# Kernel optimization log

Measured on AMD Instinct MI355X. Metric: run time of the kernel, lower is better.

The kernel has to match this reference:

```python
import jax, jax.numpy as jnp
import numpy as np

IMAGE_SIZE = 800.0          # torchvision default min_size
SCORE_THRESH = 0.25         # box_score_thresh from __init__
NMS_THRESH = 0.5            # box_nms_thresh from __init__
MAX_DET = 100               # torchvision detections_per_img default
BBOX_XFORM_CLIP = float(np.log(1000.0 / 16.0))  # torchvision BoxCoder clamp


def setup_inputs() -> dict:
    key = jax.random.key(0)
    k = jax.random.split(key, 5)
    B, N, D, C = 16, 4000, 1024, 2
    feats = jax.random.normal(k[0], (B, N, D), dtype=jnp.float32)
    # valid proposal boxes (x1,y1,x2,y2) inside the image
    cxcy = jax.random.uniform(k[1], (B, N, 2), minval=64.0, maxval=IMAGE_SIZE - 64.0)
    wh = jax.random.uniform(k[2], (B, N, 2), minval=16.0, maxval=128.0)
    proposals = jnp.concatenate([cxcy - wh * 0.5, cxcy + wh * 0.5], axis=-1)
    W_cls = jax.random.normal(k[3], (C, D), dtype=jnp.float32) * 0.02
    b_cls = jnp.zeros((C,), jnp.float32)
    W_box = jax.random.normal(k[4], (C * 4, D), dtype=jnp.float32) * 0.01
    b_box = jnp.zeros((C * 4,), jnp.float32)
    return dict(feats=feats, proposals=proposals, W_cls=W_cls, b_cls=b_cls,
                W_box=W_box, b_box=b_box)


def _decode_boxes(deltas, proposals):
    # torchvision BoxCoder with weights (10, 10, 5, 5)
    wx, wy, ww, wh = 10.0, 10.0, 5.0, 5.0
    widths = proposals[..., 2] - proposals[..., 0]
    heights = proposals[..., 3] - proposals[..., 1]
    ctr_x = proposals[..., 0] + 0.5 * widths
    ctr_y = proposals[..., 1] + 0.5 * heights
    dx = deltas[..., 0] / wx
    dy = deltas[..., 1] / wy
    dw = jnp.minimum(deltas[..., 2] / ww, BBOX_XFORM_CLIP)
    dh = jnp.minimum(deltas[..., 3] / wh, BBOX_XFORM_CLIP)
    pcx = dx * widths + ctr_x
    pcy = dy * heights + ctr_y
    pw = jnp.exp(dw) * widths
    ph = jnp.exp(dh) * heights
    boxes = jnp.stack([pcx - 0.5 * pw, pcy - 0.5 * ph,
                       pcx + 0.5 * pw, pcy + 0.5 * ph], axis=-1)
    return jnp.clip(boxes, 0.0, IMAGE_SIZE)


def _nms_keep(boxes, scores):
    # greedy NMS for one image; boxes [N,4], scores [N] (already thresholded)
    areas = jnp.maximum(boxes[:, 2] - boxes[:, 0], 0.0) * \
            jnp.maximum(boxes[:, 3] - boxes[:, 1], 0.0)

    def body(carry, _):
        s, keep = carry
        i = jnp.argmax(s)
        valid = s[i] > 0.0
        bi = boxes[i]
        ix1 = jnp.maximum(bi[0], boxes[:, 0])
        iy1 = jnp.maximum(bi[1], boxes[:, 1])
        ix2 = jnp.minimum(bi[2], boxes[:, 2])
        iy2 = jnp.minimum(bi[3], boxes[:, 3])
        inter = jnp.maximum(ix2 - ix1, 0.0) * jnp.maximum(iy2 - iy1, 0.0)
        iou = inter / (areas[i] + areas - inter + 1e-9)
        s = jnp.where(iou > NMS_THRESH, 0.0, s).at[i].set(0.0)
        keep = keep.at[i].set(valid)
        return (s, keep), None

    init = (scores, jnp.zeros(scores.shape, dtype=bool))
    (_, keep), _ = jax.lax.scan(body, init, None, length=MAX_DET)
    return keep


def reference(feats, proposals, W_cls, b_cls, W_box, b_box):
    logits = jnp.einsum('bnd,cd->bnc', feats, W_cls) + b_cls       # [B,N,2]
    deltas = jnp.einsum('bnd,ed->bne', feats, W_box) + b_box       # [B,N,8]
    probs = jax.nn.softmax(logits, axis=-1)
    scores = probs[..., 1]                                          # foreground class
    fg_deltas = deltas[..., 4:8]                                    # class-1 deltas
    boxes = _decode_boxes(fg_deltas, proposals)                     # [B,N,4]
    scores = jnp.where(scores > SCORE_THRESH, scores, 0.0)
    keep = jax.vmap(_nms_keep)(boxes, scores)                       # [B,N] bool
    final_scores = scores * keep.astype(scores.dtype)
    return jnp.concatenate([boxes, final_scores[..., None]], axis=-1)  # [B,N,5]
```

## Files before the change

kernel.cpp:

```cpp
#include <hip/hip_runtime.h>
#include <math.h>

#define IMG 800.0f
#define SCORE_TH 0.25f
#define NMS_TH 0.5f
#define MAXDET 100
#define BBOX_CLIP 4.135166556742356f

constexpr int kB = 16;
constexpr int kN = 4000;
constexpr int kD = 1024;

__global__ __launch_bounds__(256, 2) void head_kernel(
    const float* __restrict__ feats, const float* __restrict__ proposals,
    const float* __restrict__ Wc, const float* __restrict__ bc,
    const float* __restrict__ Wb, const float* __restrict__ bb,
    float* __restrict__ out, float* __restrict__ ws_scores,
    float* __restrict__ ws_boxes) {
  const int lane = threadIdx.x & 63;
  const int waveId = (blockIdx.x * blockDim.x + threadIdx.x) >> 6;
  const int nWaves = (gridDim.x * blockDim.x) >> 6;

  const float4* Wc4 = (const float4*)Wc;
  const float4* Wb4 = (const float4*)Wb;
  float4 w0[4], w1[4], w4[4], w5[4], w6[4], w7[4];
#pragma unroll
  for (int ch = 0; ch < 4; ++ch) {
    int idx = ch * 64 + lane;
    w0[ch] = Wc4[0 * 256 + idx];
    w1[ch] = Wc4[1 * 256 + idx];
    w4[ch] = Wb4[4 * 256 + idx];
    w5[ch] = Wb4[5 * 256 + idx];
    w6[ch] = Wb4[6 * 256 + idx];
    w7[ch] = Wb4[7 * 256 + idx];
  }
  const float bc0 = bc[0], bc1 = bc[1];
  const float bb4 = bb[4], bb5 = bb[5], bb6 = bb[6], bb7 = bb[7];

  const int R = kB * kN;
  for (int row = waveId; row < R; row += nWaves) {
    const float4* F = (const float4*)(feats + (size_t)row * kD);
    float a0 = 0.f, a1 = 0.f, a4 = 0.f, a5 = 0.f, a6 = 0.f, a7 = 0.f;
#pragma unroll
    for (int ch = 0; ch < 4; ++ch) {
      float4 f = F[ch * 64 + lane];
      a0 = fmaf(f.x, w0[ch].x, fmaf(f.y, w0[ch].y, fmaf(f.z, w0[ch].z, fmaf(f.w, w0[ch].w, a0))));
      a1 = fmaf(f.x, w1[ch].x, fmaf(f.y, w1[ch].y, fmaf(f.z, w1[ch].z, fmaf(f.w, w1[ch].w, a1))));
      a4 = fmaf(f.x, w4[ch].x, fmaf(f.y, w4[ch].y, fmaf(f.z, w4[ch].z, fmaf(f.w, w4[ch].w, a4))));
      a5 = fmaf(f.x, w5[ch].x, fmaf(f.y, w5[ch].y, fmaf(f.z, w5[ch].z, fmaf(f.w, w5[ch].w, a5))));
      a6 = fmaf(f.x, w6[ch].x, fmaf(f.y, w6[ch].y, fmaf(f.z, w6[ch].z, fmaf(f.w, w6[ch].w, a6))));
      a7 = fmaf(f.x, w7[ch].x, fmaf(f.y, w7[ch].y, fmaf(f.z, w7[ch].z, fmaf(f.w, w7[ch].w, a7))));
    }
#pragma unroll
    for (int off = 32; off; off >>= 1) {
      a0 += __shfl_xor(a0, off);
      a1 += __shfl_xor(a1, off);
      a4 += __shfl_xor(a4, off);
      a5 += __shfl_xor(a5, off);
      a6 += __shfl_xor(a6, off);
      a7 += __shfl_xor(a7, off);
    }
    if (lane == 0) {
      float l0 = a0 + bc0, l1 = a1 + bc1;
      float score = 1.0f / (1.0f + __expf(l0 - l1));
      float sth = score > SCORE_TH ? score : 0.0f;

      float4 p = ((const float4*)proposals)[row];
      float w = p.z - p.x, h = p.w - p.y;
      float cx = p.x + 0.5f * w, cy = p.y + 0.5f * h;
      float dx = (a4 + bb4) * 0.1f;
      float dy = (a5 + bb5) * 0.1f;
      float dw = fminf((a6 + bb6) * 0.2f, BBOX_CLIP);
      float dh = fminf((a7 + bb7) * 0.2f, BBOX_CLIP);
      float pcx = fmaf(dx, w, cx), pcy = fmaf(dy, h, cy);
      float pw = __expf(dw) * w, ph = __expf(dh) * h;
      float x1 = fminf(fmaxf(pcx - 0.5f * pw, 0.f), IMG);
      float y1 = fminf(fmaxf(pcy - 0.5f * ph, 0.f), IMG);
      float x2 = fminf(fmaxf(pcx + 0.5f * pw, 0.f), IMG);
      float y2 = fminf(fmaxf(pcy + 0.5f * ph, 0.f), IMG);

      size_t ob = (size_t)row * 5;
      out[ob + 0] = x1;
      out[ob + 1] = y1;
      out[ob + 2] = x2;
      out[ob + 3] = y2;
      ws_scores[row] = sth;
      ((float4*)ws_boxes)[row] = make_float4(x1, y1, x2, y2);
    }
  }
}

template <int CTRL>
__device__ __forceinline__ unsigned long long dpp_max_u64(unsigned long long k) {
  int lo = __builtin_amdgcn_update_dpp(0, (int)(unsigned)k, CTRL, 0xF, 0xF, true);
  int hi =
      __builtin_amdgcn_update_dpp(0, (int)(unsigned)(k >> 32), CTRL, 0xF, 0xF, true);
  unsigned long long o = ((unsigned long long)(unsigned)hi << 32) | (unsigned)lo;
  return o > k ? o : k;
}

__device__ __forceinline__ unsigned long long wave_max_u64(unsigned long long k) {
  k = dpp_max_u64<0x121>(k);
  k = dpp_max_u64<0x122>(k);
  k = dpp_max_u64<0x124>(k);
  k = dpp_max_u64<0x128>(k);
  k = dpp_max_u64<0x142>(k);
  k = dpp_max_u64<0x143>(k);
  return k;
}

__global__ __launch_bounds__(256, 1) void nms_kernel(
    const float* __restrict__ ws_scores, const float* __restrict__ ws_boxes,
    float* __restrict__ out) {
  const int b = blockIdx.x;
  const int t = threadIdx.x;
  const int wave = t >> 6;
  const int lane = t & 63;

  __shared__ float4 Lbox[kN];
  __shared__ unsigned long long Lkey[2][4];

  const float* sc = ws_scores + (size_t)b * kN;
  const float4* bx = (const float4*)ws_boxes + (size_t)b * kN;

  unsigned khi[16];
  float areaE[16];
  float4 box[16];
  unsigned keep_mask = 0u;
  const unsigned nt = ~(unsigned)t;

#pragma unroll
  for (int k = 0; k < 16; ++k) {
    int n = k * 256 + t;
    if (n < kN) {
      box[k] = bx[n];
      khi[k] = __float_as_uint(sc[n]);
      areaE[k] = fmaxf(box[k].z - box[k].x, 0.f) *
                     fmaxf(box[k].w - box[k].y, 0.f) +
                 1e-9f;
      Lbox[n] = box[k];
    } else {
      box[k] = make_float4(0.f, 0.f, 0.f, 0.f);
      khi[k] = 0u;
      areaE[k] = 1e-9f;
    }
  }

  auto reduce_publish = [&](int parity) {
    unsigned long long lk[16];
#pragma unroll
    for (int k = 0; k < 16; ++k)
      lk[k] = ((unsigned long long)khi[k] << 32) |
              (unsigned long long)(nt - (unsigned)(k * 256));
#pragma unroll
    for (int k = 0; k < 8; ++k) lk[k] = lk[k] > lk[k + 8] ? lk[k] : lk[k + 8];
#pragma unroll
    for (int k = 0; k < 4; ++k) lk[k] = lk[k] > lk[k + 4] ? lk[k] : lk[k + 4];
    lk[0] = lk[0] > lk[2] ? lk[0] : lk[2];
    lk[1] = lk[1] > lk[3] ? lk[1] : lk[3];
    lk[0] = lk[0] > lk[1] ? lk[0] : lk[1];
    unsigned long long wkey = wave_max_u64(lk[0]);
    if (lane == 63) Lkey[parity][wave] = wkey;
  };

  reduce_publish(1);
  __syncthreads();

  for (int it = 0; it < MAXDET; ++it) {
    const int pr = (it + 1) & 1;
    unsigned long long wk = Lkey[pr][0];
    unsigned long long k1 = Lkey[pr][1];
    unsigned long long k2 = Lkey[pr][2];
    unsigned long long k3 = Lkey[pr][3];
    wk = wk > k1 ? wk : k1;
    k2 = k2 > k3 ? k2 : k3;
    wk = wk > k2 ? wk : k2;
    const unsigned whi = (unsigned)__builtin_amdgcn_readfirstlane((int)(wk >> 32));
    const unsigned wlo = (unsigned)__builtin_amdgcn_readfirstlane((int)(unsigned)wk);
    const unsigned wn = ~wlo;
    const bool valid = whi != 0u;
    const float4 wb = Lbox[wn];
    const float wa = fmaxf(wb.z - wb.x, 0.f) * fmaxf(wb.w - wb.y, 0.f);
    const bool iOwn = ((unsigned)t == (wn & 255u));
    const int oSlot = (int)(wn >> 8);
    if (iOwn) {
      unsigned bit = 1u << oSlot;
      keep_mask = valid ? (keep_mask | bit) : (keep_mask & ~bit);
    }
#pragma unroll
    for (int k = 0; k < 16; ++k) {
      float dx = fminf(wb.z, box[k].z) - fmaxf(wb.x, box[k].x);
      float dy = fminf(wb.w, box[k].w) - fmaxf(wb.y, box[k].y);
      float inter3 = 3.0f * fmaxf(dx, 0.f) * fmaxf(dy, 0.f);
      bool sup = inter3 > wa + areaE[k];
      if (sup || (iOwn && k == oSlot)) khi[k] = 0u;
    }
    reduce_publish(it & 1);
    __syncthreads();
  }

#pragma unroll
  for (int k = 0; k < 16; ++k) {
    int n = k * 256 + t;
    if (n < kN) {
      out[((size_t)(b * kN + n)) * 5 + 4] =
          (keep_mask >> k) & 1u ? sc[n] : 0.0f;
    }
  }
}

extern "C" void kernel_launch(void* const* d_in, const int* in_sizes, int n_in,
                              void* d_out, int out_size, void* d_ws,
                              size_t ws_size, hipStream_t stream) {
  const float* feats = (const float*)d_in[0];
  const float* proposals = (const float*)d_in[1];
  const float* Wc = (const float*)d_in[2];
  const float* bc = (const float*)d_in[3];
  const float* Wb = (const float*)d_in[4];
  const float* bb = (const float*)d_in[5];
  float* out = (float*)d_out;

  float* ws_scores = (float*)d_ws;
  float* ws_boxes = ws_scores + kB * kN;

  head_kernel<<<512, 256, 0, stream>>>(feats, proposals, Wc, bc, Wb, bb, out,
                                       ws_scores, ws_boxes);
  nms_kernel<<<kB, 256, 0, stream>>>(ws_scores, ws_boxes, out);
}
```

Baseline: 444.6 us.

## Widen NMS blocks to 512 threads and publish winner boxes per wave

The NMS kernel now runs 512 threads per image, so each thread holds 8 candidates instead of 16. Each wave publishes its winning box alongside its key, which removes the full shared-memory box array and its indexed lookup. The wave max reduction uses DPP within rows followed by readlane instead of the cross-row DPP steps. Scores are kept as packed 64-bit keys to avoid rebuilding them on every iteration. The cost is a longer reduction across 8 wave slots and a block barrier spanning more waves.

```diff
diff --git a/kernel.cpp b/kernel.cpp
--- a/kernel.cpp
+++ b/kernel.cpp
@@ -10,6 +10,8 @@
 constexpr int kB = 16;
 constexpr int kN = 4000;
 constexpr int kD = 1024;
+
+typedef unsigned long long ull;
 
 __global__ __launch_bounds__(256, 2) void head_kernel(
     const float* __restrict__ feats, const float* __restrict__ proposals,
@@ -91,25 +93,20 @@
 }
 
 template <int CTRL>
-__device__ __forceinline__ unsigned long long dpp_max_u64(unsigned long long k) {
+__device__ __forceinline__ ull dpp_max_u64(ull k) {
   int lo = __builtin_amdgcn_update_dpp(0, (int)(unsigned)k, CTRL, 0xF, 0xF, true);
-  int hi =
-      __builtin_amdgcn_update_dpp(0, (int)(unsigned)(k >> 32), CTRL, 0xF, 0xF, true);
-  unsigned long long o = ((unsigned long long)(unsigned)hi << 32) | (unsigned)lo;
+  int hi = __builtin_amdgcn_update_dpp(0, (int)(unsigned)(k >> 32), CTRL, 0xF, 0xF, true);
+  ull o = ((ull)(unsigned)hi << 32) | (unsigned)lo;
   return o > k ? o : k;
 }
 
-__device__ __forceinline__ unsigned long long wave_max_u64(unsigned long long k) {
-  k = dpp_max_u64<0x121>(k);
-  k = dpp_max_u64<0x122>(k);
-  k = dpp_max_u64<0x124>(k);
-  k = dpp_max_u64<0x128>(k);
-  k = dpp_max_u64<0x142>(k);
-  k = dpp_max_u64<0x143>(k);
-  return k;
-}
-
-__global__ __launch_bounds__(256, 1) void nms_kernel(
+__device__ __forceinline__ ull read_lane_u64(ull v, int lane) {
+  unsigned lo = (unsigned)__builtin_amdgcn_readlane((int)(unsigned)v, lane);
+  unsigned hi = (unsigned)__builtin_amdgcn_readlane((int)(v >> 32), lane);
+  return ((ull)hi << 32) | lo;
+}
+
+__global__ __launch_bounds__(512, 2) void nms_kernel(
     const float* __restrict__ ws_scores, const float* __restrict__ ws_boxes,
     float* __restrict__ out) {
   const int b = blockIdx.x;
@@ -117,50 +114,60 @@
   const int wave = t >> 6;
   const int lane = t & 63;
 
-  __shared__ float4 Lbox[kN];
-  __shared__ unsigned long long Lkey[2][4];
+  __shared__ ull Lkey[2][8];
+  __shared__ float4 LboxW[2][8];
 
   const float* sc = ws_scores + (size_t)b * kN;
   const float4* bx = (const float4*)ws_boxes + (size_t)b * kN;
 
-  unsigned khi[16];
-  float areaE[16];
-  float4 box[16];
+  ull key[8];
+  float areaE[8];
+  float4 box[8];
   unsigned keep_mask = 0u;
   const unsigned nt = ~(unsigned)t;
 
 #pragma unroll
-  for (int k = 0; k < 16; ++k) {
-    int n = k * 256 + t;
+  for (int k = 0; k < 8; ++k) {
+    int n = k * 512 + t;
+    unsigned lo = nt - (unsigned)(k << 9);
     if (n < kN) {
       box[k] = bx[n];
-      khi[k] = __float_as_uint(sc[n]);
+      key[k] = ((ull)__float_as_uint(sc[n]) << 32) | lo;
       areaE[k] = fmaxf(box[k].z - box[k].x, 0.f) *
                      fmaxf(box[k].w - box[k].y, 0.f) +
                  1e-9f;
-      Lbox[n] = box[k];
     } else {
       box[k] = make_float4(0.f, 0.f, 0.f, 0.f);
-      khi[k] = 0u;
+      key[k] = (ull)lo;
       areaE[k] = 1e-9f;
     }
   }
 
   auto reduce_publish = [&](int parity) {
-    unsigned long long lk[16];
-#pragma unroll
-    for (int k = 0; k < 16; ++k)
-      lk[k] = ((unsigned long long)khi[k] << 32) |
-              (unsigned long long)(nt - (unsigned)(k * 256));
-#pragma unroll
-    for (int k = 0; k < 8; ++k) lk[k] = lk[k] > lk[k + 8] ? lk[k] : lk[k + 8];
-#pragma unroll
-    for (int k = 0; k < 4; ++k) lk[k] = lk[k] > lk[k + 4] ? lk[k] : lk[k + 4];
-    lk[0] = lk[0] > lk[2] ? lk[0] : lk[2];
-    lk[1] = lk[1] > lk[3] ? lk[1] : lk[3];
-    lk[0] = lk[0] > lk[1] ? lk[0] : lk[1];
-    unsigned long long wkey = wave_max_u64(lk[0]);
-    if (lane == 63) Lkey[parity][wave] = wkey;
+    ull m = key[0];
+#pragma unroll
+    for (int k = 1; k < 8; ++k) m = key[k] > m ? key[k] : m;
+    const ull lk = m;
+    m = dpp_max_u64<0x121>(m);
+    m = dpp_max_u64<0x122>(m);
+    m = dpp_max_u64<0x124>(m);
+    m = dpp_max_u64<0x128>(m);
+    ull r0 = read_lane_u64(m, 0);
+    ull r1 = read_lane_u64(m, 16);
+    ull r2 = read_lane_u64(m, 32);
+    ull r3 = read_lane_u64(m, 48);
+    r0 = r1 > r0 ? r1 : r0;
+    r2 = r3 > r2 ? r3 : r2;
+    r0 = r2 > r0 ? r2 : r0;
+    if (lk == r0) {
+      unsigned n = ~(unsigned)r0;
+      int slot = n >> 9;
+      float4 sb = box[0];
+#pragma unroll
+      for (int k = 1; k < 8; ++k) sb = (slot == k) ? box[k] : sb;
+      Lkey[parity][wave] = r0;
+      LboxW[parity][wave] = sb;
+    }
   };
 
   reduce_publish(1);
@@ -168,40 +175,43 @@
 
   for (int it = 0; it < MAXDET; ++it) {
     const int pr = (it + 1) & 1;
-    unsigned long long wk = Lkey[pr][0];
-    unsigned long long k1 = Lkey[pr][1];
-    unsigned long long k2 = Lkey[pr][2];
-    unsigned long long k3 = Lkey[pr][3];
-    wk = wk > k1 ? wk : k1;
-    k2 = k2 > k3 ? k2 : k3;
-    wk = wk > k2 ? wk : k2;
-    const unsigned whi = (unsigned)__builtin_amdgcn_readfirstlane((int)(wk >> 32));
-    const unsigned wlo = (unsigned)__builtin_amdgcn_readfirstlane((int)(unsigned)wk);
+    ull k0 = Lkey[pr][0], k1 = Lkey[pr][1], k2 = Lkey[pr][2], k3 = Lkey[pr][3];
+    ull k4 = Lkey[pr][4], k5 = Lkey[pr][5], k6 = Lkey[pr][6], k7 = Lkey[pr][7];
+    k0 = k1 > k0 ? k1 : k0;
+    k2 = k3 > k2 ? k3 : k2;
+    k4 = k5 > k4 ? k5 : k4;
+    k6 = k7 > k6 ? k7 : k6;
+    k0 = k2 > k0 ? k2 : k0;
+    k4 = k6 > k4 ? k6 : k4;
+    k0 = k4 > k0 ? k4 : k0;
+    const unsigned whi = (unsigned)__builtin_amdgcn_readfirstlane((int)(k0 >> 32));
+    const unsigned wlo = (unsigned)__builtin_amdgcn_readfirstlane((int)(unsigned)k0);
     const unsigned wn = ~wlo;
     const bool valid = whi != 0u;
-    const float4 wb = Lbox[wn];
+    const int wwave = (int)((wn >> 6) & 7);
+    const float4 wb = LboxW[pr][wwave];
     const float wa = fmaxf(wb.z - wb.x, 0.f) * fmaxf(wb.w - wb.y, 0.f);
-    const bool iOwn = ((unsigned)t == (wn & 255u));
-    const int oSlot = (int)(wn >> 8);
+    const bool iOwn = ((unsigned)t == (wn & 511u));
+    const int oSlot = (int)(wn >> 9);
     if (iOwn) {
       unsigned bit = 1u << oSlot;
       keep_mask = valid ? (keep_mask | bit) : (keep_mask & ~bit);
     }
 #pragma unroll
-    for (int k = 0; k < 16; ++k) {
+    for (int k = 0; k < 8; ++k) {
       float dx = fminf(wb.z, box[k].z) - fmaxf(wb.x, box[k].x);
       float dy = fminf(wb.w, box[k].w) - fmaxf(wb.y, box[k].y);
       float inter3 = 3.0f * fmaxf(dx, 0.f) * fmaxf(dy, 0.f);
-      bool sup = inter3 > wa + areaE[k];
-      if (sup || (iOwn && k == oSlot)) khi[k] = 0u;
+      bool clr = (inter3 > wa + areaE[k]) || (iOwn && k == oSlot);
+      if (clr) key[k] &= 0xFFFFFFFFull;
     }
     reduce_publish(it & 1);
     __syncthreads();
   }
 
 #pragma unroll
-  for (int k = 0; k < 16; ++k) {
-    int n = k * 256 + t;
+  for (int k = 0; k < 8; ++k) {
+    int n = k * 512 + t;
     if (n < kN) {
       out[((size_t)(b * kN + n)) * 5 + 4] =
           (keep_mask >> k) & 1u ? sc[n] : 0.0f;
@@ -225,5 +235,5 @@
 
   head_kernel<<<512, 256, 0, stream>>>(feats, proposals, Wc, bc, Wb, bb, out,
                                        ws_scores, ws_boxes);
-  nms_kernel<<<kB, 256, 0, stream>>>(ws_scores, ws_boxes, out);
-}
+  nms_kernel<<<kB, 512, 0, stream>>>(ws_scores, ws_boxes, out);
+}
```

After: 722.2 us. 1.62x slower.
